# Optimization experiments

Measured on AMD Instinct MI355X. Metric: run time of the kernel, lower is better.

Reference implementation:

```python
import jax, jax.numpy as jnp
import numpy as np

B, S, M = 2, 2048, 2048
NQ, NKV, H = 16, 4, 128
EPS = 1e-6
MAX_WAVELENGTH = 10000.0
NEG_INF = -1e9


def rmsnorm(x, scale, eps=EPS):
    # RMSNorm over head_dim (last axis), computed in fp32.
    xf = x.astype(jnp.float32)
    var = jnp.mean(xf * xf, axis=-1, keepdims=True)
    return (xf * jax.lax.rsqrt(var + eps) * scale).astype(x.dtype)


def rope(x, max_wavelength=MAX_WAVELENGTH, scaling_factor=1.0, start_index=0):
    # x: [b, s, n, h]; keras_hub split-half rotary embedding.
    h = x.shape[-1]
    inv_freq = 1.0 / (max_wavelength ** (jnp.arange(0, h, 2, dtype=jnp.float32) / h))
    pos = (jnp.arange(x.shape[1], dtype=jnp.float32) + start_index) / scaling_factor
    freq = pos[:, None] * inv_freq[None, :]             # [s, h/2]
    emb = jnp.concatenate([freq, freq], axis=-1)        # [s, h]
    cos = jnp.cos(emb)[None, :, None, :]
    sin = jnp.sin(emb)[None, :, None, :]
    x1, x2 = x[..., : h // 2], x[..., h // 2 :]
    rot = jnp.concatenate([-x2, x1], axis=-1)
    return (x * cos + rot * sin).astype(x.dtype)


def setup_inputs() -> dict:
    key = jax.random.key(0)
    ks = jax.random.split(key, 6)
    hidden_states = jax.random.normal(ks[0], (B, S, M), dtype=jnp.float32)
    # causal mask [b, q, k]
    causal = jnp.tril(jnp.ones((S, S), dtype=bool))
    attention_mask = jnp.broadcast_to(causal[None], (B, S, S))
    sq = 0.02
    Wq = jax.random.normal(ks[1], (M, NQ, H), dtype=jnp.float32) * sq
    Wk = jax.random.normal(ks[2], (M, NKV, H), dtype=jnp.float32) * sq
    Wv = jax.random.normal(ks[3], (M, NKV, H), dtype=jnp.float32) * sq
    Wo = jax.random.normal(ks[4], (NQ, H, M), dtype=jnp.float32) * sq
    q_scale = jnp.ones((H,), dtype=jnp.float32)
    k_scale = jnp.ones((H,), dtype=jnp.float32)
    return {
        "hidden_states": hidden_states,
        "attention_mask": attention_mask,
        "Wq": Wq,
        "Wk": Wk,
        "Wv": Wv,
        "Wo": Wo,
        "q_scale": q_scale,
        "k_scale": k_scale,
    }


def reference(hidden_states, attention_mask, Wq, Wk, Wv, Wo, q_scale, k_scale):
    inv_norm = 1.0 / np.sqrt(H)
    groups = NQ // NKV

    q = jnp.einsum("bqm,muh->bquh", hidden_states, Wq)   # [b,q,NQ,H]
    q = rope(rmsnorm(q, q_scale))
    k = jnp.einsum("bkm,mvh->bkvh", hidden_states, Wk)   # [b,k,NKV,H]
    k = rope(rmsnorm(k, k_scale))
    v = jnp.einsum("bkm,mvh->bkvh", hidden_states, Wv)

    # GQA broadcast: repeat each kv head `groups` times consecutively.
    k = jnp.repeat(k, groups, axis=2)
    v = jnp.repeat(v, groups, axis=2)

    scores = jnp.einsum("bquh,bkuh->buqk", q, k) * inv_norm  # [b,u,q,k]
    scores = scores.astype(jnp.float32)
    scores = jnp.where(attention_mask[:, None, :, :], scores, NEG_INF)
    probs = jax.nn.softmax(scores, axis=-1).astype(hidden_states.dtype)

    attn = jnp.einsum("buqk,bkuh->bquh", probs, v)
    out = jnp.einsum("bquh,uhm->bqm", attn, Wo)
    return out
```

## Files before the change

kernel.cpp:

```cpp
#include <hip/hip_runtime.h>
#include <stdint.h>

#define BB 2
#define SS 2048
#define MM 2048
#define NQ 16
#define NKV 4
#define HH 128
#define KVB 64

typedef __attribute__((ext_vector_type(4))) float f32x4;
typedef __attribute__((ext_vector_type(16))) float f32x16;
typedef _Float16 f16x8 __attribute__((ext_vector_type(8)));
typedef _Float16 f16x4 __attribute__((ext_vector_type(4)));
typedef _Float16 f16x2 __attribute__((ext_vector_type(2)));
typedef unsigned int uint4v __attribute__((ext_vector_type(4)));

__device__ __forceinline__ void gll16(const _Float16* g, _Float16* l) {
  __builtin_amdgcn_global_load_lds(
      (__attribute__((address_space(1))) void*)g,
      (__attribute__((address_space(3))) void*)l, 16, 0, 0);
}

__global__ __launch_bounds__(256) void k_f32_to_f16(const float* __restrict__ in,
                                                    _Float16* __restrict__ out, int n4) {
  int i = blockIdx.x * 256 + threadIdx.x;
  if (i >= n4) return;
  float4 v = ((const float4*)in)[i];
  f16x4 o = { (_Float16)v.x, (_Float16)v.y, (_Float16)v.z, (_Float16)v.w };
  ((f16x4*)out)[i] = o;
}

__global__ __launch_bounds__(256) void k_wtrans(
    const float* __restrict__ Wq, const float* __restrict__ Wk,
    const float* __restrict__ Wv, const float* __restrict__ Wo,
    _Float16* __restrict__ Wqkvt, _Float16* __restrict__ Wot) {
  const int z = blockIdx.z;
  if ((z == 1 || z == 2) && blockIdx.y >= 16) return;
  const float* in = (z == 0) ? Wq : (z == 1) ? Wk : (z == 2) ? Wv : Wo;
  _Float16* out = (z == 3) ? Wot : Wqkvt;
  const int N_in = (z == 1 || z == 2) ? 512 : 2048;
  const int n_off = (z == 1) ? 2048 : (z == 2) ? 2560 : 0;

  __shared__ float tile[32][33];
  const int k0 = blockIdx.x * 32;
  const int n0 = blockIdx.y * 32;
  const int tx = threadIdx.x & 31;
  const int ty = threadIdx.x >> 5;
  #pragma unroll
  for (int r = ty; r < 32; r += 8)
    tile[r][tx] = in[(size_t)(k0 + r) * N_in + n0 + tx];
  __syncthreads();
  #pragma unroll
  for (int r = ty; r < 32; r += 8)
    out[(size_t)(n0 + r + n_off) * 2048 + k0 + tx] = (_Float16)tile[tx][r];
}

__global__ __launch_bounds__(256) void k_vtrans(const _Float16* __restrict__ qkv,
                                                _Float16* __restrict__ VtG) {
  __shared__ _Float16 tile[32][33];
  const int s0 = blockIdx.x * 32;
  const int z = blockIdx.y;
  const int h0 = (z & 3) * 32;
  const int bv = z >> 2;
  const int b = bv >> 2;
  const int hv = bv & 3;
  const int tx = threadIdx.x & 31;
  const int ty = threadIdx.x >> 5;
  #pragma unroll
  for (int r = ty; r < 32; r += 8)
    tile[r][tx] = qkv[(size_t)(b * SS + s0 + r) * 3072 + 2560 + hv * 128 + h0 + tx];
  __syncthreads();
  #pragma unroll
  for (int r = ty; r < 32; r += 8)
    VtG[((size_t)bv * HH + h0 + r) * SS + s0 + tx] = tile[tx][r];
}

template <int FN, bool F16OUT>
__global__ __launch_bounds__(512, 2) void k_gemm256(
    const _Float16* __restrict__ A, const _Float16* __restrict__ Bt,
    void* __restrict__ Cout, int NT_M, int N, int K) {
  __shared__ _Float16 As[2][256 * 64];
  __shared__ _Float16 Bs[2][FN * 64 * 64];

  const int tid = threadIdx.x;
  const int w = tid >> 6;
  const int l = tid & 63;
  const int lr = l & 15;
  const int al4 = l >> 4;
  const int wr = w >> 2;
  const int wc = w & 3;
  const int swz = (lr & 7) << 4;

  const int nwg = gridDim.x;
  const int bid = blockIdx.x;
  const int sbid = (bid & 7) * (nwg >> 3) + (bid >> 3);
  const int bm = (sbid % NT_M) * 256;
  const int bn = (sbid / NT_M) * (FN * 64);
  const int KT = K >> 6;

  const int srow = tid >> 3;
  const int sch = (tid & 7) ^ (srow & 7);
  const _Float16* aSrc = A + (size_t)(bm + srow) * K + sch * 8;
  const _Float16* bSrc = Bt + (size_t)(bn + srow) * K + sch * 8;

  auto stA = [&](int buf, int r, int kt) {
    gll16(aSrc + (size_t)(r * 64) * K + kt * 64, &As[buf][r * 4096 + w * 512]);
  };
  auto stB = [&](int buf, int r, int kt) {
    gll16(bSrc + (size_t)(r * 64) * K + kt * 64, &Bs[buf][r * 4096 + w * 512]);
  };

  f32x4 acc[8][FN] = {};

  stA(0, 0, 0); stA(0, 1, 0); stA(0, 2, 0); stA(0, 3, 0);
  stB(0, 0, 0); stB(0, 1, 0);
  if (FN == 3) stB(0, 2, 0);
  if (KT > 1) {
    stA(1, 0, 1); stA(1, 2, 1); stB(1, 0, 1); stB(1, 1, 1);
    asm volatile("s_waitcnt vmcnt(4)" ::: "memory");
  } else {
    asm volatile("s_waitcnt vmcnt(0)" ::: "memory");
  }
  __builtin_amdgcn_s_barrier();

  for (int t = 0; t < KT; ++t) {
    const int cb = t & 1;
    const char* Ab = (const char*)&As[cb][0];
    const char* Bb = (const char*)&Bs[cb][0];
    f16x8 bF[FN][2];
    #pragma unroll
    for (int ph = 0; ph < 4; ++ph) {
      f16x8 aF[2][2];
      #pragma unroll
      for (int fm = 0; fm < 2; ++fm)
        #pragma unroll
        for (int ks = 0; ks < 2; ++ks) {
          const int row = wr * 128 + (ph * 2 + fm) * 16 + lr;
          aF[fm][ks] = *(const f16x8*)(Ab + row * 128 + (((ks * 4 + al4) * 16) ^ swz));
        }
      if (ph == 0) {
        #pragma unroll
        for (int fn = 0; fn < FN; ++fn)
          #pragma unroll
          for (int ks = 0; ks < 2; ++ks) {
            const int col = wc * (FN * 16) + fn * 16 + lr;
            bF[fn][ks] = *(const f16x8*)(Bb + col * 128 + (((ks * 4 + al4) * 16) ^ swz));
          }
      }
      if (ph == 0 && FN == 3 && t + 1 < KT) stB(cb ^ 1, 2, t + 1);
      if (ph == 1 && t + 1 < KT) { stA(cb ^ 1, 1, t + 1); stA(cb ^ 1, 3, t + 1); }
      if (ph == 2 && t + 2 < KT) { stA(cb, 0, t + 2); stA(cb, 2, t + 2); }
      if (ph == 3 && t + 2 < KT) { stB(cb, 0, t + 2); stB(cb, 1, t + 2); }
      __builtin_amdgcn_s_barrier();
      asm volatile("s_waitcnt lgkmcnt(0)" ::: "memory");
      __builtin_amdgcn_sched_barrier(0);
      __builtin_amdgcn_s_setprio(1);
      #pragma unroll
      for (int fm = 0; fm < 2; ++fm)
        #pragma unroll
        for (int fn = 0; fn < FN; ++fn)
          #pragma unroll
          for (int ks = 0; ks < 2; ++ks)
            acc[ph * 2 + fm][fn] = __builtin_amdgcn_mfma_f32_16x16x32_f16(
                aF[fm][ks], bF[fn][ks], acc[ph * 2 + fm][fn], 0, 0, 0);
      __builtin_amdgcn_s_setprio(0);
      __builtin_amdgcn_sched_barrier(0);
      if (ph < 3) {
        __builtin_amdgcn_s_barrier();
      } else {
        if (t + 2 < KT) asm volatile("s_waitcnt vmcnt(4)" ::: "memory");
        else            asm volatile("s_waitcnt vmcnt(0)" ::: "memory");
        __builtin_amdgcn_s_barrier();
      }
    }
  }

  #pragma unroll
  for (int fm = 0; fm < 8; ++fm) {
    #pragma unroll
    for (int i = 0; i < 4; ++i) {
      const int row = bm + wr * 128 + fm * 16 + al4 * 4 + i;
      #pragma unroll
      for (int fn = 0; fn < FN; ++fn) {
        const int col = bn + wc * (FN * 16) + fn * 16 + lr;
        if (F16OUT)
          ((_Float16*)Cout)[(size_t)row * N + col] = (_Float16)acc[fm][fn][i];
        else
          ((float*)Cout)[(size_t)row * N + col] = acc[fm][fn][i];
      }
    }
  }
}

__global__ __launch_bounds__(256) void k_normrope(
    const _Float16* __restrict__ qkv,
    const float* __restrict__ q_scale, const float* __restrict__ k_scale,
    _Float16* __restrict__ Qr, _Float16* __restrict__ Kr) {
  const int row = blockIdx.x;
  const int b = row >> 11;
  const int s = row & 2047;
  const int hh = blockIdx.y * 4 + (threadIdx.x >> 6);
  const int l = threadIdx.x & 63;
  const _Float16* src = qkv + (size_t)row * 3072 + hh * 128 + l * 2;
  float x0 = (float)src[0];
  float x1 = (float)src[1];
  float ssum = x0 * x0 + x1 * x1;
  #pragma unroll
  for (int d = 1; d < 64; d <<= 1) ssum += __shfl_xor(ssum, d);
  const float rstd = rsqrtf(ssum * (1.f / 128.f) + 1e-6f);
  const float* scl = (hh < 16) ? q_scale : k_scale;
  x0 *= rstd * scl[2 * l];
  x1 *= rstd * scl[2 * l + 1];
  const float y0 = __shfl_xor(x0, 32);
  const float y1 = __shfl_xor(x1, 32);
  const int j0 = (2 * l) & 63;
  const float kLog = 0.20762050593046014f;
  const float f0 = (float)s * exp2f(-(float)j0 * kLog);
  const float f1 = (float)s * exp2f(-(float)(j0 + 1) * kLog);
  const float c0 = cosf(f0), s0 = sinf(f0);
  const float c1 = cosf(f1), s1 = sinf(f1);
  float r0, r1;
  if (l < 32) { r0 = x0 * c0 - y0 * s0; r1 = x1 * c1 - y1 * s1; }
  else        { r0 = x0 * c0 + y0 * s0; r1 = x1 * c1 + y1 * s1; }
  if (hh < 16) {
    _Float16* dst = Qr + ((size_t)(b * NQ + hh) * SS + s) * HH + 2 * l;
    dst[0] = (_Float16)r0; dst[1] = (_Float16)r1;
  } else {
    _Float16* dst = Kr + ((size_t)(b * NKV + (hh - 16)) * SS + s) * HH + 2 * l;
    dst[0] = (_Float16)r0; dst[1] = (_Float16)r1;
  }
}

__device__ const unsigned char g_tasks[24] = {
  61, 63, 28,
  57, 59, 53, 55, 24,
  49, 51, 45, 47, 20,
  41, 43, 37, 39, 16,
  33, 35, 12,
  8, 4, 0
};

__global__ __launch_bounds__(256, 2) void k_attn(
    const _Float16* __restrict__ Qr, const _Float16* __restrict__ Kr,
    const _Float16* __restrict__ VtG,
    const float* __restrict__ qs, const float* __restrict__ ks,
    float* __restrict__ PartA, float* __restrict__ PartB,
    float* __restrict__ psA, float* __restrict__ psB,
    _Float16* __restrict__ Ao) {
  __shared__ _Float16 Ks[2][KVB * 128];
  __shared__ _Float16 Vs[2][128 * KVB];

  const int tid = threadIdx.x;
  const int w = tid >> 6;
  const int l = tid & 63;
  const int l31 = l & 31;
  const int hi = l >> 5;
  const int sw7 = (l31 & 7) << 4;
  const int bu = blockIdx.x;
  const int b = bu >> 4, u = bu & 15;
  const int kvh = u >> 2;

  const int task = g_tasks[blockIdx.y];
  const int heavy = task & 1;
  const int half = (task >> 1) & 1;
  const int qt = task >> 2;
  const int q0 = qt * 128;
  const int halfLen = qt + 1;
  const int t0 = heavy ? half * halfLen : 0;
  const int t1 = heavy ? t0 + halfLen : 2 * qt + 2;

  float ma = fmaxf(fabsf(qs[l]), fabsf(qs[l + 64]));
  float mb = fmaxf(fabsf(ks[l]), fabsf(ks[l + 64]));
  #pragma unroll
  for (int d = 1; d < 64; d <<= 1) {
    ma = fmaxf(ma, __shfl_xor(ma, d));
    mb = fmaxf(mb, __shfl_xor(mb, d));
  }
  const float M2 = 1.4426950408889634f * ma * mb;
  const float K2 = 0.12752982260735795f;

  const _Float16* Kbase = Kr + (size_t)(b * NKV + kvh) * SS * HH;
  const _Float16* Vbase = VtG + (size_t)(b * NKV + kvh) * HH * SS;

  f16x8 qf[8];
  {
    const _Float16* qp = Qr + ((size_t)(b * NQ + u) * SS + q0 + w * 32 + l31) * HH + hi * 8;
    #pragma unroll
    for (int hs = 0; hs < 8; hs++) {
      qf[hs] = *(const f16x8*)(qp + hs * 16);
      qf[hs] *= (_Float16)K2;
    }
  }

  f32x16 acc0 = {}, acc1 = {}, acc2 = {}, acc3 = {};
  float psum = 0.f;

  auto stage = [&](int buf, int t) {
    const int kv0 = t * KVB;
    #pragma unroll
    for (int it = 0; it < 4; it++) {
      const int n = it * 256 + tid;
      {
        const int row = n >> 4, c = n & 15;
        const int cs = c ^ (row & 7);
        gll16(Kbase + (size_t)(kv0 + row) * HH + cs * 8,
              &Ks[buf][(size_t)(it * 256 + w * 64) * 8]);
      }
      {
        const int row = n >> 3, c = n & 7;
        const int cs = c ^ (row & 7);
        gll16(Vbase + (size_t)row * SS + kv0 + cs * 8,
              &Vs[buf][(size_t)(it * 256 + w * 64) * 8]);
      }
    }
  };

  int buf = 0;
  stage(0, t0);
  __syncthreads();

  const int qwb = q0 + w * 32;
  const int qlane = qwb + l31;

  for (int t = t0; t < t1; t++) {
    if (t + 1 < t1) stage(buf ^ 1, t + 1);
    const int kv0 = t * KVB;
    if (kv0 <= qwb + 31) {
      const char* Kb = (const char*)&Ks[buf][0];
      const char* Vb = (const char*)&Vs[buf][0];

      f32x16 S0 = {}, S1 = {};
      __builtin_amdgcn_s_setprio(1);
      #pragma unroll
      for (int hs = 0; hs < 8; hs++) {
        const int ch = hs * 2 + hi;
        f16x8 k0 = *(const f16x8*)(Kb + l31 * 256 + ((ch << 4) ^ sw7));
        f16x8 k1 = *(const f16x8*)(Kb + (32 + l31) * 256 + ((ch << 4) ^ sw7));
        S0 = __builtin_amdgcn_mfma_f32_32x32x16_f16(k0, qf[hs], S0, 0, 0, 0);
        S1 = __builtin_amdgcn_mfma_f32_32x32x16_f16(k1, qf[hs], S1, 0, 0, 0);
      }
      __builtin_amdgcn_s_setprio(0);

      const bool domask = (kv0 + 63 > qwb);
      float p0[16], p1[16];
      #pragma unroll
      for (int r = 0; r < 16; r++) {
        const int cr = (r & 3) + 8 * (r >> 2) + 4 * hi;
        float e0 = exp2f(S0[r] - M2);
        float e1 = exp2f(S1[r] - M2);
        if (domask) {
          if (kv0 + cr > qlane) e0 = 0.f;
          if (kv0 + 32 + cr > qlane) e1 = 0.f;
        }
        p0[r] = e0; p1[r] = e1;
        psum += e0 + e1;
      }

      unsigned int pkv[4][4];
      #pragma unroll
      for (int g = 0; g < 4; g++) {
        f16x2 ha = { (_Float16)p0[2 * g], (_Float16)p0[2 * g + 1] };
        f16x2 hb = { (_Float16)p0[8 + 2 * g], (_Float16)p0[9 + 2 * g] };
        f16x2 hc = { (_Float16)p1[2 * g], (_Float16)p1[2 * g + 1] };
        f16x2 hd = { (_Float16)p1[8 + 2 * g], (_Float16)p1[9 + 2 * g] };
        pkv[0][g] = __builtin_bit_cast(unsigned int, ha);
        pkv[1][g] = __builtin_bit_cast(unsigned int, hb);
        pkv[2][g] = __builtin_bit_cast(unsigned int, hc);
        pkv[3][g] = __builtin_bit_cast(unsigned int, hd);
      }
      f16x8 pa[4];
      #pragma unroll
      for (int ksx = 0; ksx < 4; ksx++) {
        unsigned int a0 = pkv[ksx][0], a1 = pkv[ksx][1], a2 = pkv[ksx][2], a3 = pkv[ksx][3];
        unsigned int x0 = (unsigned int)__shfl_xor((int)a0, 32);
        unsigned int x1 = (unsigned int)__shfl_xor((int)a1, 32);
        unsigned int x2 = (unsigned int)__shfl_xor((int)a2, 32);
        unsigned int x3 = (unsigned int)__shfl_xor((int)a3, 32);
        uint4v dv;
        dv.x = hi ? x2 : a0;
        dv.y = hi ? x3 : a1;
        dv.z = hi ? a2 : x0;
        dv.w = hi ? a3 : x1;
        pa[ksx] = __builtin_bit_cast(f16x8, dv);
      }

      __builtin_amdgcn_s_setprio(1);
      #pragma unroll
      for (int ksx = 0; ksx < 4; ksx++) {
        const int ch = ksx * 2 + hi;
        f16x8 v0 = *(const f16x8*)(Vb + (0 * 32 + l31) * 128 + ((ch << 4) ^ sw7));
        acc0 = __builtin_amdgcn_mfma_f32_32x32x16_f16(pa[ksx], v0, acc0, 0, 0, 0);
        f16x8 v1 = *(const f16x8*)(Vb + (1 * 32 + l31) * 128 + ((ch << 4) ^ sw7));
        acc1 = __builtin_amdgcn_mfma_f32_32x32x16_f16(pa[ksx], v1, acc1, 0, 0, 0);
        f16x8 v2 = *(const f16x8*)(Vb + (2 * 32 + l31) * 128 + ((ch << 4) ^ sw7));
        acc2 = __builtin_amdgcn_mfma_f32_32x32x16_f16(pa[ksx], v2, acc2, 0, 0, 0);
        f16x8 v3 = *(const f16x8*)(Vb + (3 * 32 + l31) * 128 + ((ch << 4) ^ sw7));
        acc3 = __builtin_amdgcn_mfma_f32_32x32x16_f16(pa[ksx], v3, acc3, 0, 0, 0);
      }
      __builtin_amdgcn_s_setprio(0);
    }
    __syncthreads();
    buf ^= 1;
  }

  const float tot = psum + __shfl_xor(psum, 32);
  if (heavy) {
    const int slot = bu * 8 + (qt - 8);
    float* pPart = (half ? PartB : PartA) + (size_t)slot * 16384;
    float* sPart = (half ? psB : psA) + slot * 128;
    if (hi == 0) sPart[w * 32 + l31] = tot;
    #pragma unroll
    for (int r = 0; r < 16; r++) {
      const int cr = (r & 3) + 8 * (r >> 2) + 4 * hi;
      float* dst = pPart + (size_t)(w * 32 + cr) * 128 + l31;
      dst[0]  = acc0[r];
      dst[32] = acc1[r];
      dst[64] = acc2[r];
      dst[96] = acc3[r];
    }
  } else {
    const float inv = 1.f / tot;
    #pragma unroll
    for (int r = 0; r < 16; r++) {
      const int cr = (r & 3) + 8 * (r >> 2) + 4 * hi;
      const float ivr = __shfl(inv, cr);
      _Float16* dst = Ao + ((size_t)(b * SS + q0 + w * 32 + cr)) * MM + u * HH + l31;
      dst[0]  = (_Float16)(acc0[r] * ivr);
      dst[32] = (_Float16)(acc1[r] * ivr);
      dst[64] = (_Float16)(acc2[r] * ivr);
      dst[96] = (_Float16)(acc3[r] * ivr);
    }
  }
}

__global__ __launch_bounds__(256) void k_fin(
    const float* __restrict__ PartA, const float* __restrict__ PartB,
    const float* __restrict__ psA, const float* __restrict__ psB,
    _Float16* __restrict__ Ao) {
  const int slot = blockIdx.x;
  const int bu = slot >> 3, st = slot & 7;
  const int b = bu >> 4, u = bu & 15;
  const int qt = st + 8;
  const float* pa = PartA + (size_t)slot * 16384;
  const float* pb = PartB + (size_t)slot * 16384;
  const float* sa = psA + slot * 128;
  const float* sb = psB + slot * 128;
  #pragma unroll
  for (int it = 0; it < 16; it++) {
    const int unit = it * 256 + threadIdx.x;
    const int qr = unit >> 5, cg = unit & 31;
    const float inv = 1.f / (sa[qr] + sb[qr]);
    f32x4 va = *(const f32x4*)(pa + qr * 128 + cg * 4);
    f32x4 vb = *(const f32x4*)(pb + qr * 128 + cg * 4);
    f16x4 o = { (_Float16)((va[0] + vb[0]) * inv), (_Float16)((va[1] + vb[1]) * inv),
                (_Float16)((va[2] + vb[2]) * inv), (_Float16)((va[3] + vb[3]) * inv) };
    *(f16x4*)(Ao + ((size_t)(b * SS + qt * 128 + qr)) * MM + u * HH + cg * 4) = o;
  }
}

extern "C" void kernel_launch(void* const* d_in, const int* in_sizes, int n_in,
                              void* d_out, int out_size, void* d_ws, size_t ws_size,
                              hipStream_t stream) {
  const float* hidden = (const float*)d_in[0];
  const float* Wq = (const float*)d_in[2];
  const float* Wk = (const float*)d_in[3];
  const float* Wv = (const float*)d_in[4];
  const float* Wo = (const float*)d_in[5];
  const float* q_scale = (const float*)d_in[6];
  const float* k_scale = (const float*)d_in[7];

  char* ws = (char*)d_ws;
  _Float16* Xb    = (_Float16*)(ws);
  _Float16* Wqkvt = (_Float16*)(ws + 16777216);
  _Float16* Wot   = (_Float16*)(ws + 29360128);
  _Float16* qkv   = (_Float16*)(ws + 37748736);
  _Float16* Qr    = (_Float16*)(ws + 62914560);
  _Float16* Kr    = (_Float16*)(ws + 79691776);
  _Float16* VtG   = (_Float16*)(ws + 83886080);
  _Float16* Ao    = (_Float16*)(ws + 88080384);
  float*    PartB = (float*)(ws);
  float*    PartA = (float*)(ws + 37748736);
  float*    psA   = (float*)(ws + 54525952);
  float*    psB   = (float*)(ws + 54657024);

  k_f32_to_f16<<<dim3(8192), dim3(256), 0, stream>>>(hidden, Xb, 2097152);
  k_wtrans<<<dim3(64, 64, 4), dim3(256), 0, stream>>>(Wq, Wk, Wv, Wo, Wqkvt, Wot);
  k_gemm256<3, true><<<dim3(256), dim3(512), 0, stream>>>(Xb, Wqkvt, (void*)qkv, 16, 3072, 2048);
  k_normrope<<<dim3(4096, 5), dim3(256), 0, stream>>>(qkv, q_scale, k_scale, Qr, Kr);
  k_vtrans<<<dim3(64, 32), dim3(256), 0, stream>>>(qkv, VtG);
  k_attn<<<dim3(32, 24), dim3(256), 0, stream>>>(Qr, Kr, VtG, q_scale, k_scale,
                                                 PartA, PartB, psA, psB, Ao);
  k_fin<<<dim3(256), dim3(256), 0, stream>>>(PartA, PartB, psA, psB, Ao);
  k_gemm256<2, false><<<dim3(256), dim3(512), 0, stream>>>(Ao, Wot, d_out, 16, 2048, 2048);
}
```

Baseline: 236.9 us.

## Double attention query tile to 256 rows with 512-thread blocks

The attention kernel now handles 256 query rows per block with 8 waves instead of 128 rows with 4, so each staged K/V tile is shared by twice as many queries. The task table, the split of heavy causal tiles and the partial-result slot layout are rebuilt for the larger tile, and the finalize kernel is changed to match. This halves K/V global-to-LDS traffic per query but gives fewer, larger blocks with coarser causal load balancing and possible occupancy limits at 512 threads.

```diff
diff --git a/kernel.cpp b/kernel.cpp
--- a/kernel.cpp
+++ b/kernel.cpp
@@ -232,16 +232,11 @@
   }
 }
 
-__device__ const unsigned char g_tasks[24] = {
-  61, 63, 28,
-  57, 59, 53, 55, 24,
-  49, 51, 45, 47, 20,
-  41, 43, 37, 39, 16,
-  33, 35, 12,
-  8, 4, 0
+__device__ const unsigned char g_tasks[12] = {
+  30, 31, 12, 26, 27, 22, 23, 8, 18, 19, 4, 0
 };
 
-__global__ __launch_bounds__(256, 2) void k_attn(
+__global__ __launch_bounds__(512, 2) void k_attn(
     const _Float16* __restrict__ Qr, const _Float16* __restrict__ Kr,
     const _Float16* __restrict__ VtG,
     const float* __restrict__ qs, const float* __restrict__ ks,
@@ -262,13 +257,13 @@
   const int kvh = u >> 2;
 
   const int task = g_tasks[blockIdx.y];
-  const int heavy = task & 1;
-  const int half = (task >> 1) & 1;
-  const int qt = task >> 2;
-  const int q0 = qt * 128;
-  const int halfLen = qt + 1;
+  const int s = task >> 2;
+  const int heavy = (task >> 1) & 1;
+  const int half = task & 1;
+  const int q0 = s * 256;
+  const int halfLen = 2 * (s + 1);
   const int t0 = heavy ? half * halfLen : 0;
-  const int t1 = heavy ? t0 + halfLen : 2 * qt + 2;
+  const int t1 = heavy ? t0 + halfLen : 4 * (s + 1);
 
   float ma = fmaxf(fabsf(qs[l]), fabsf(qs[l + 64]));
   float mb = fmaxf(fabsf(ks[l]), fabsf(ks[l + 64]));
@@ -299,19 +294,19 @@
   auto stage = [&](int buf, int t) {
     const int kv0 = t * KVB;
     #pragma unroll
-    for (int it = 0; it < 4; it++) {
-      const int n = it * 256 + tid;
+    for (int it = 0; it < 2; it++) {
+      const int n = it * 512 + tid;
       {
         const int row = n >> 4, c = n & 15;
         const int cs = c ^ (row & 7);
         gll16(Kbase + (size_t)(kv0 + row) * HH + cs * 8,
-              &Ks[buf][(size_t)(it * 256 + w * 64) * 8]);
+              &Ks[buf][(size_t)(it * 512 + w * 64) * 8]);
       }
       {
         const int row = n >> 3, c = n & 7;
         const int cs = c ^ (row & 7);
         gll16(Vbase + (size_t)row * SS + kv0 + cs * 8,
-              &Vs[buf][(size_t)(it * 256 + w * 64) * 8]);
+              &Vs[buf][(size_t)(it * 512 + w * 64) * 8]);
       }
     }
   };
@@ -406,9 +401,9 @@
 
   const float tot = psum + __shfl_xor(psum, 32);
   if (heavy) {
-    const int slot = bu * 8 + (qt - 8);
-    float* pPart = (half ? PartB : PartA) + (size_t)slot * 16384;
-    float* sPart = (half ? psB : psA) + slot * 128;
+    const int slot = bu * 4 + (s - 4);
+    float* pPart = (half ? PartB : PartA) + (size_t)slot * 32768;
+    float* sPart = (half ? psB : psA) + slot * 256;
     if (hi == 0) sPart[w * 32 + l31] = tot;
     #pragma unroll
     for (int r = 0; r < 16; r++) {
@@ -438,14 +433,15 @@
     const float* __restrict__ PartA, const float* __restrict__ PartB,
     const float* __restrict__ psA, const float* __restrict__ psB,
     _Float16* __restrict__ Ao) {
-  const int slot = blockIdx.x;
-  const int bu = slot >> 3, st = slot & 7;
+  const int bx = blockIdx.x;
+  const int slot = bx >> 1, qh = bx & 1;
+  const int bu = slot >> 2, st = slot & 3;
   const int b = bu >> 4, u = bu & 15;
-  const int qt = st + 8;
-  const float* pa = PartA + (size_t)slot * 16384;
-  const float* pb = PartB + (size_t)slot * 16384;
-  const float* sa = psA + slot * 128;
-  const float* sb = psB + slot * 128;
+  const int q0 = (st + 4) * 256 + qh * 128;
+  const float* pa = PartA + (size_t)slot * 32768 + qh * 16384;
+  const float* pb = PartB + (size_t)slot * 32768 + qh * 16384;
+  const float* sa = psA + slot * 256 + qh * 128;
+  const float* sb = psB + slot * 256 + qh * 128;
   #pragma unroll
   for (int it = 0; it < 16; it++) {
     const int unit = it * 256 + threadIdx.x;
@@ -455,7 +451,7 @@
     f32x4 vb = *(const f32x4*)(pb + qr * 128 + cg * 4);
     f16x4 o = { (_Float16)((va[0] + vb[0]) * inv), (_Float16)((va[1] + vb[1]) * inv),
                 (_Float16)((va[2] + vb[2]) * inv), (_Float16)((va[3] + vb[3]) * inv) };
-    *(f16x4*)(Ao + ((size_t)(b * SS + qt * 128 + qr)) * MM + u * HH + cg * 4) = o;
+    *(f16x4*)(Ao + ((size_t)(b * SS + q0 + qr)) * MM + u * HH + cg * 4) = o;
   }
 }
 
@@ -489,7 +485,7 @@
   k_gemm256<3, true><<<dim3(256), dim3(512), 0, stream>>>(Xb, Wqkvt, (void*)qkv, 16, 3072, 2048);
   k_normrope<<<dim3(4096, 5), dim3(256), 0, stream>>>(qkv, q_scale, k_scale, Qr, Kr);
   k_vtrans<<<dim3(64, 32), dim3(256), 0, stream>>>(qkv, VtG);
-  k_attn<<<dim3(32, 24), dim3(256), 0, stream>>>(Qr, Kr, VtG, q_scale, k_scale,
+  k_attn<<<dim3(32, 12), dim3(512), 0, stream>>>(Qr, Kr, VtG, q_scale, k_scale,
                                                  PartA, PartB, psA, psB, Ao);
   k_fin<<<dim3(256), dim3(256), 0, stream>>>(PartA, PartB, psA, psB, Ao);
   k_gemm256<2, false><<<dim3(256), dim3(512), 0, stream>>>(Ao, Wot, d_out, 16, 2048, 2048);
```

Result: slower. 244.0 us (+3.0%).
